# Performance work log

Hardware: AMD Instinct MI355X
Metric: run time of the kernel (lower is better)

The kernel has to match this reference:

```python
import jax, jax.numpy as jnp
import numpy as np
import math

B, L, H, NH = 4, 2048, 2048, 16
HD = H // NH  # head_dim = 128
ROPE_BASE = 10000.0


def rotate_half(x):
    x1, x2 = jnp.split(x, 2, axis=-1)
    return jnp.concatenate((-x2, x1), axis=-1)


def rope_cos_sin(seq_len, dim, dtype=jnp.float32):
    inv_freq = 1.0 / (ROPE_BASE ** (jnp.arange(0, dim, 2, dtype=jnp.float32) / dim))
    t = jnp.arange(seq_len, dtype=jnp.float32)
    freqs = jnp.outer(t, inv_freq)              # [L, dim/2]
    emb = jnp.concatenate((freqs, freqs), -1)   # [L, dim]
    return jnp.cos(emb).astype(dtype), jnp.sin(emb).astype(dtype)


def setup_inputs() -> dict:
    key = jax.random.key(0)
    ks = jax.random.split(key, 5)
    x = jax.random.normal(ks[0], (B, L, H), dtype=jnp.float32)
    # causal mask, broadcastable over [B, NH, L, L]; 0 -> masked
    mask = jnp.tril(jnp.ones((L, L), dtype=jnp.int32))[None, None]
    s = 0.02
    Wq = jax.random.normal(ks[1], (H, H), dtype=jnp.float32) * s
    Wk = jax.random.normal(ks[2], (H, H), dtype=jnp.float32) * s
    Wv = jax.random.normal(ks[3], (H, H), dtype=jnp.float32) * s
    Wo = jax.random.normal(ks[4], (H, H), dtype=jnp.float32) * s
    return {"x": x, "mask": mask, "Wq": Wq, "Wk": Wk, "Wv": Wv, "Wo": Wo}


def reference(x, mask, Wq, Wk, Wv, Wo):
    b, l, _ = x.shape
    # nn.Linear: y = x @ W.T (weight shape [out, in])
    q = (x @ Wq.T).reshape(b, l, NH, HD).transpose(0, 2, 1, 3)  # [B,H,L,D]
    k = (x @ Wk.T).reshape(b, l, NH, HD).transpose(0, 2, 1, 3)
    v = (x @ Wv.T).reshape(b, l, NH, HD).transpose(0, 2, 1, 3)
    cos, sin = rope_cos_sin(l, HD, x.dtype)  # [L, D] broadcasts over [B,H,L,D]
    q = q * cos + rotate_half(q) * sin
    k = k * cos + rotate_half(k) * sin
    attn = jnp.einsum("bhqd,bhkd->bhqk", q, k) / math.sqrt(HD)
    attn = jnp.where(mask == 0, jnp.float32(-jnp.inf), attn)
    attn = jax.nn.softmax(attn.astype(jnp.float32), axis=-1).astype(x.dtype)
    out = jnp.einsum("bhqk,bhkd->bhqd", attn, v)
    out = out.transpose(0, 2, 1, 3).reshape(b, l, NH * HD)
    return out @ Wo.T
```

## Files before the change

kernel.cpp:

```cpp
#include <hip/hip_runtime.h>
#include <cstdint>
#include <cmath>

#define B_   4
#define L_   2048
#define H_   2048
#define NH_  16
#define HD_  128
#define ML_  (B_*L_)

using short8 = __attribute__((ext_vector_type(8))) short;
using f32x4  = __attribute__((ext_vector_type(4))) float;
using f32x16 = __attribute__((ext_vector_type(16))) float;
using uint4v = __attribute__((ext_vector_type(4))) unsigned;

__device__ inline short f2bf(float f){
  unsigned u = __builtin_bit_cast(unsigned, f);
  unsigned r = u + 0x7FFFu + ((u >> 16) & 1u);
  return (short)(r >> 16);
}
__device__ inline float bf2f(short s){
  unsigned u = ((unsigned)(unsigned short)s) << 16;
  return __builtin_bit_cast(float, u);
}

#define GLD16(gp, lp) __builtin_amdgcn_global_load_lds(                      \
    (const __attribute__((address_space(1))) void*)(gp),                     \
    (__attribute__((address_space(3))) void*)(lp), 16, 0, 0)

__device__ inline unsigned cvtpk_bf16(float lo, float hi){
  unsigned d;
  asm("v_cvt_pk_bf16_f32 %0, %1, %2" : "=v"(d) : "v"(lo), "v"(hi));
  return d;
}
__device__ inline void permswap32(unsigned &a, unsigned &b){
  asm volatile("v_permlane32_swap_b32 %0, %1" : "+v"(a), "+v"(b));
}
__device__ inline float cross_half_max(float x){
  return fmaxf(x, __shfl_xor(x, 32));
}
__device__ inline float cross_half_add(float x){
  return x + __shfl_xor(x, 32);
}

__global__ void rope_table(float* __restrict__ cosT, float* __restrict__ sinT){
  int idx = blockIdx.x * 256 + threadIdx.x;
  if (idx >= L_ * 64) return;
  int l = idx >> 6, d = idx & 63;
  float invf = powf(10000.0f, -(float)d * (1.0f/64.0f));
  float fr = (float)l * invf;
  cosT[idx] = cosf(fr);
  sinT[idx] = sinf(fr);
}

__global__ __launch_bounds__(256)
void cvt_bf16(const float* __restrict__ in, short* __restrict__ out, int n8){
  int i = blockIdx.x * 256 + threadIdx.x;
  if (i >= n8) return;
  const float4* p = (const float4*)(in + (size_t)i * 8);
  float4 a = p[0], b = p[1];
  short8 s;
  s[0]=f2bf(a.x); s[1]=f2bf(a.y); s[2]=f2bf(a.z); s[3]=f2bf(a.w);
  s[4]=f2bf(b.x); s[5]=f2bf(b.y); s[6]=f2bf(b.z); s[7]=f2bf(b.w);
  *(short8*)(out + (size_t)i * 8) = s;
}

__global__ __launch_bounds__(256)
void cvt_w3(const float* __restrict__ W0, const float* __restrict__ W1,
            const float* __restrict__ W2, short* __restrict__ out){
  int i = blockIdx.x * 256 + threadIdx.x;
  const int per = H_ * H_ / 8;
  const float* src; int j;
  if (i < per)            { src = W0; j = i; }
  else if (i < 2 * per)   { src = W1; j = i - per; }
  else                    { src = W2; j = i - 2 * per; }
  const float4* p = (const float4*)(src + (size_t)j * 8);
  float4 a = p[0], b = p[1];
  short8 s;
  s[0]=f2bf(a.x); s[1]=f2bf(a.y); s[2]=f2bf(a.z); s[3]=f2bf(a.w);
  s[4]=f2bf(b.x); s[5]=f2bf(b.y); s[6]=f2bf(b.z); s[7]=f2bf(b.w);
  *(short8*)(out + (size_t)i * 8) = s;
}

template<int QKV, int OUT_F32>
__global__ __launch_bounds__(512, 2)
void gemm256_bt(const short* __restrict__ A, const short* __restrict__ Bw,
                void* __restrict__ C0, void* __restrict__ C1,
                void* __restrict__ C2)
{
  constexpr int K = 2048, N = 2048;
  __shared__ short sA[4][256 * 32];
  __shared__ short sB[4][256 * 32];
  const int tid  = threadIdx.x;
  const int lane = tid & 63;
  const int wave = tid >> 6;
  const int wr = wave >> 2, wc = wave & 3;
  const int ln = lane & 15, g = lane >> 4;

  const int blk = blockIdx.x;
  int n_t, m_t;
  if constexpr (QKV) { int i = blk >> 3; n_t = (blk & 7) + 8 * (i >> 5); m_t = i & 31; }
  else               { n_t = blk & 7;    m_t = blk >> 3; }
  const int m0 = m_t * 256;
  const int nb0 = n_t * 256;

  const int u0 = wave * 64 + lane;
  const int u1 = u0 + 512;
  const int r0 = u0 >> 2, c0 = (((u0 & 3) ^ (r0 & 3) ^ ((r0 >> 2) & 3))) * 8;
  const int r1 = u1 >> 2, c1 = (((u1 & 3) ^ (r1 & 3) ^ ((r1 >> 2) & 3))) * 8;

  f32x4 acc[8][4];
  #pragma unroll
  for (int m = 0; m < 8; m++)
    #pragma unroll
    for (int n = 0; n < 4; n++) acc[m][n] = {0.f, 0.f, 0.f, 0.f};

#define STAGE256(T) do {                                                     \
    const int _b = (T) & 3; const int _k = (T) * 32;                         \
    GLD16(A  + (size_t)(m0 + r0) * K + _k + c0, &sA[_b][wave * 512]);        \
    GLD16(A  + (size_t)(m0 + r1) * K + _k + c1, &sA[_b][4096 + wave * 512]); \
    GLD16(Bw + (size_t)(nb0 + r0) * K + _k + c0, &sB[_b][wave * 512]);       \
    GLD16(Bw + (size_t)(nb0 + r1) * K + _k + c1, &sB[_b][4096 + wave * 512]);\
  } while (0)

#define TILE256(T, VMN, PF) do {                                             \
    asm volatile("s_waitcnt vmcnt(" #VMN ")" ::: "memory");                  \
    __builtin_amdgcn_s_barrier();                                            \
    asm volatile("" ::: "memory");                                           \
    const short* _at = &sA[(T) & 3][0];                                      \
    const short* _bt = &sB[(T) & 3][0];                                      \
    short8 af[8], bfr[4];                                                    \
    const int _sl = (g ^ (ln & 3) ^ ((ln >> 2) & 3)) * 8;                    \
    _Pragma("unroll")                                                        \
    for (int m = 0; m < 8; m++)                                              \
      af[m] = *(const short8*)(_at + (wr * 128 + m * 16 + ln) * 32 + _sl);   \
    _Pragma("unroll")                                                        \
    for (int n = 0; n < 4; n++)                                              \
      bfr[n] = *(const short8*)(_bt + (wc * 64 + n * 16 + ln) * 32 + _sl);   \
    if (PF) STAGE256((T) + 3);                                               \
    __builtin_amdgcn_s_setprio(1);                                           \
    _Pragma("unroll")                                                        \
    for (int m = 0; m < 8; m++)                                              \
      _Pragma("unroll")                                                      \
      for (int n = 0; n < 4; n++)                                            \
        acc[m][n] = __builtin_amdgcn_mfma_f32_16x16x32_bf16(af[m], bfr[n],   \
                                                            acc[m][n], 0, 0, 0); \
    __builtin_amdgcn_s_setprio(0);                                           \
  } while (0)

  STAGE256(0); STAGE256(1); STAGE256(2);

  for (int t = 0; t < 61; ++t) TILE256(t, 8, true);
  TILE256(61, 8, false);
  TILE256(62, 4, false);
  TILE256(63, 0, false);

#undef STAGE256
#undef TILE256

  void* Cp; int cb;
  if constexpr (QKV) {
    int w = n_t >> 3;
    Cp = (w == 0) ? C0 : (w == 1) ? C1 : C2;
    cb = (n_t & 7) * 256;
  } else { Cp = C0; cb = nb0; }
  #pragma unroll
  for (int m = 0; m < 8; m++)
    #pragma unroll
    for (int n = 0; n < 4; n++)
      #pragma unroll
      for (int r = 0; r < 4; r++) {
        int row = m0 + wr * 128 + m * 16 + g * 4 + r;
        int col = cb + wc * 64 + n * 16 + ln;
        float v = acc[m][n][r];
        if constexpr (OUT_F32) ((float*)Cp)[(size_t)row * N + col] = v;
        else                   ((short*)Cp)[(size_t)row * N + col] = f2bf(v);
      }
}

__global__ __launch_bounds__(256)
void rope_apply(short* __restrict__ Qb, short* __restrict__ Kb,
                const float* __restrict__ cosT, const float* __restrict__ sinT)
{
  int idx = blockIdx.x * 256 + threadIdx.x;
  int z = blockIdx.y;
  short* ptr  = z ? Kb : Qb;
  float scale = z ? 1.0f : 0.08838834764831845f;
  int row = idx >> 7;
  int rem = idx & 127;
  int h = rem >> 3, ch = rem & 7;
  int l = row & (L_ - 1);
  short* base = ptr + (size_t)row * H_ + h * HD_ + ch * 8;
  short8 lo = *(short8*)base;
  short8 hi = *(short8*)(base + 64);
  const float* cp = cosT + l * 64 + ch * 8;
  const float* sp = sinT + l * 64 + ch * 8;
  short8 nlo, nhi;
  #pragma unroll
  for (int j = 0; j < 8; j++) {
    float c = cp[j], s = sp[j];
    float x0 = bf2f(lo[j]), x1 = bf2f(hi[j]);
    nlo[j] = f2bf((x0 * c - x1 * s) * scale);
    nhi[j] = f2bf((x1 * c + x0 * s) * scale);
  }
  *(short8*)base        = nlo;
  *(short8*)(base + 64) = nhi;
}

__global__ __launch_bounds__(256)
void transpose_v(const short* __restrict__ Vb, short* __restrict__ VT)
{
  __shared__ short t[64 * 64];
  const int blk = blockIdx.x;
  const int dt = blk & 1, lt = (blk >> 1) & 31, bh = blk >> 6;
  const int b = bh >> 4, h = bh & 15;
  const int l0 = lt * 64, d0 = dt * 64;
  const int tid = threadIdx.x;
  #pragma unroll
  for (int i = 0; i < 2; i++) {
    int u = tid + i * 256;
    int r = u >> 3, c = u & 7;
    short8 v = *(const short8*)(Vb + ((size_t)b * L_ + l0 + r) * H_ + h * HD_ + d0 + c * 8);
    *(short8*)&t[r * 64 + ((c ^ ((r >> 3) & 7)) << 3)] = v;
  }
  __syncthreads();
  #pragma unroll
  for (int i = 0; i < 2; i++) {
    int u = tid + i * 256;
    int d = u >> 3, lc = u & 7;
    short8 o;
    #pragma unroll
    for (int j = 0; j < 8; j++) {
      int l = lc * 8 + j;
      o[j] = t[l * 64 + (((d >> 3) ^ (lc & 7)) << 3) + (d & 7)];
    }
    *(short8*)(VT + ((size_t)bh * HD_ + d0 + d) * L_ + l0 + lc * 8) = o;
  }
}

__global__ __launch_bounds__(512, 2)
void flash_attn(const short* __restrict__ Qb, const short* __restrict__ Kb,
                const short* __restrict__ VT, short* __restrict__ AO)
{
  __shared__ short lds_k[2][64 * 128];
  __shared__ short lds_v[2][128 * 64];
  __shared__ float f_lds[8][32];

  const int blk = blockIdx.x;
  int bh, j;
  if (blk < 256) { bh = blk & 63; j = 7 - (blk >> 6); }
  else           { int u = blk - 256; bh = u & 63; j = 3 - (u >> 6); }
  const int q0 = j * 256;
  const int T  = 4 * j + 4;
  const int h = bh & 15, b = bh >> 4;
  const int tid = threadIdx.x, wave = tid >> 6, lane = tid & 63;
  const int hi = lane >> 5, l31 = lane & 31;
  const size_t rowbase = (size_t)b * L_;
  const int colbase = h * HD_;
  const short* Kbh  = Kb + rowbase * H_ + colbase;
  const short* VTbh = VT + (size_t)bh * HD_ * L_;
  const int qw = q0 + wave * 32;
  const int qabs = qw + l31;
  const int fsw = (l31 & 7) ^ ((l31 >> 3) & 3);

  short8 qf[8];
  {
    const short* qp = Qb + (rowbase + qabs) * H_ + colbase + hi * 8;
    #pragma unroll
    for (int c = 0; c < 8; c++) qf[c] = *(const short8*)(qp + c * 16);
  }

  f32x16 acc_o[4];
  #pragma unroll
  for (int d = 0; d < 4; d++)
    #pragma unroll
    for (int r = 0; r < 16; r++) acc_o[d][r] = 0.f;
  float m_ = -__builtin_inff(), l_ = 0.f;

  auto stage = [&](int k0s, int bufi) {
    #pragma unroll
    for (int i = 0; i < 2; i++) {
      int c = wave * 2 + i;
      {
        int rt = c * 4 + (lane >> 4);
        int cg = (lane & 15) ^ (rt & 7) ^ ((rt >> 3) & 3);
        const short* gp = Kbh + (size_t)(k0s + rt) * H_ + cg * 8;
        GLD16(gp, &lds_k[bufi][c * 512]);
      }
      {
        int rd = c * 8 + (lane >> 3);
        int cg = (lane & 7) ^ (rd & 7) ^ ((rd >> 3) & 3);
        const short* gp = VTbh + (size_t)rd * L_ + k0s + cg * 8;
        GLD16(gp, &lds_v[bufi][c * 512]);
      }
    }
  };

  stage(0, 0);
  __syncthreads();

  for (int t = 0; t < T; ++t) {
    const int k0 = t * 64;
    if (t + 1 < T) stage((t + 1) * 64, (t + 1) & 1);
    const short* kb_ = lds_k[t & 1];
    const short* vb_ = lds_v[t & 1];

    if (k0 <= qw + 31) {
      f32x16 p0, p1;
      #pragma unroll
      for (int r = 0; r < 16; r++) { p0[r] = 0.f; p1[r] = 0.f; }
      __builtin_amdgcn_s_setprio(1);
      #pragma unroll
      for (int c = 0; c < 8; c++) {
        int ch = (c * 2 + hi) ^ fsw;
        short8 kf0 = *(const short8*)(kb_ + l31 * 128 + ch * 8);
        short8 kf1 = *(const short8*)(kb_ + (32 + l31) * 128 + ch * 8);
        p0 = __builtin_amdgcn_mfma_f32_32x32x16_bf16(kf0, qf[c], p0, 0, 0, 0);
        p1 = __builtin_amdgcn_mfma_f32_32x32x16_bf16(kf1, qf[c], p1, 0, 0, 0);
      }
      __builtin_amdgcn_s_setprio(0);

      if (k0 + 63 > qw) {
        #pragma unroll
        for (int r = 0; r < 16; r++) {
          int kvl = (r & 3) + 8 * (r >> 2) + 4 * hi;
          if (k0 + kvl > qabs)      p0[r] = -__builtin_inff();
          if (k0 + 32 + kvl > qabs) p1[r] = -__builtin_inff();
        }
      }

      float mt = p0[0];
      #pragma unroll
      for (int r = 1; r < 16; r++) mt = fmaxf(mt, p0[r]);
      #pragma unroll
      for (int r = 0; r < 16; r++) mt = fmaxf(mt, p1[r]);
      mt = cross_half_max(mt);
      if (!__all(mt <= m_ + 8.0f)) {
        float mnew = fmaxf(m_, mt);
        float f = __expf(m_ - mnew);
        m_ = mnew;
        l_ *= f;
        if (lane < 32) f_lds[wave][lane] = f;
        f32x4 fr[4];
        #pragma unroll
        for (int i = 0; i < 4; i++)
          fr[i] = *(const f32x4*)&f_lds[wave][i * 8 + hi * 4];
        #pragma unroll
        for (int d = 0; d < 4; d++)
          #pragma unroll
          for (int r = 0; r < 16; r++) acc_o[d][r] *= fr[r >> 2][r & 3];
      }
      float ls = 0.f;
      #pragma unroll
      for (int r = 0; r < 16; r++) { p0[r] = __expf(p0[r] - m_); ls += p0[r]; }
      #pragma unroll
      for (int r = 0; r < 16; r++) { p1[r] = __expf(p1[r] - m_); ls += p1[r]; }
      ls = cross_half_add(ls);
      l_ += ls;

      __builtin_amdgcn_s_setprio(1);
      #pragma unroll
      for (int ks = 0; ks < 4; ks++) {
        const f32x16 &pp = (ks < 2) ? p0 : p1;
        const int kk = (ks & 1) * 8;
        unsigned a0 = cvtpk_bf16(pp[kk + 0], pp[kk + 1]);
        unsigned b0 = cvtpk_bf16(pp[kk + 4], pp[kk + 5]);
        permswap32(a0, b0);
        unsigned a1 = cvtpk_bf16(pp[kk + 2], pp[kk + 3]);
        unsigned b1 = cvtpk_bf16(pp[kk + 6], pp[kk + 7]);
        permswap32(a1, b1);
        uint4v w; w[0] = a0; w[1] = a1; w[2] = b0; w[3] = b1;
        short8 af = __builtin_bit_cast(short8, w);
        #pragma unroll
        for (int db = 0; db < 4; db++) {
          int d  = db * 32 + l31;
          int ch = (ks * 2 + hi) ^ fsw;
          short8 vf = *(const short8*)(vb_ + d * 64 + ch * 8);
          acc_o[db] = __builtin_amdgcn_mfma_f32_32x32x16_bf16(af, vf, acc_o[db], 0, 0, 0);
        }
      }
      __builtin_amdgcn_s_setprio(0);
    }
    __syncthreads();
  }

  if (lane < 32) f_lds[wave][lane] = 1.0f / l_;
  f32x4 lr[4];
  #pragma unroll
  for (int i = 0; i < 4; i++)
    lr[i] = *(const f32x4*)&f_lds[wave][i * 8 + hi * 4];
  #pragma unroll
  for (int db = 0; db < 4; db++)
    #pragma unroll
    for (int r = 0; r < 16; r++) {
      int row = qw + (r & 3) + 8 * (r >> 2) + 4 * hi;
      AO[(rowbase + row) * H_ + colbase + db * 32 + l31] =
          f2bf(acc_o[db][r] * lr[r >> 2][r & 3]);
    }
}

extern "C" void kernel_launch(void* const* d_in, const int* in_sizes, int n_in,
                              void* d_out, int out_size, void* d_ws, size_t ws_size,
                              hipStream_t stream)
{
  const float* x  = (const float*)d_in[0];
  const float* Wq = (const float*)d_in[2];
  const float* Wk = (const float*)d_in[3];
  const float* Wv = (const float*)d_in[4];
  const float* Wo = (const float*)d_in[5];
  float* out = (float*)d_out;

  char* ws = (char*)d_ws;
  const size_t SZ = (size_t)ML_ * H_ * sizeof(short);
  short* Qb = (short*)(ws);
  short* Kb = (short*)(ws + SZ);
  short* Vb = (short*)(ws + 2 * SZ);
  short* xb = (short*)(ws + 3 * SZ);
  short* VT = xb;
  short* AO = Vb;
  float* cosT = (float*)(ws + 4 * SZ);
  float* sinT = cosT + (size_t)L_ * 64;
  short* Wb = (short*)(ws + 4 * SZ + (size_t)(1 << 20));
  const size_t NEED_FUSED = 4 * SZ + (1 << 20) + (size_t)3 * H_ * H_ * sizeof(short);
  const bool fused = ws_size >= NEED_FUSED;

  rope_table<<<512, 256, 0, stream>>>(cosT, sinT);

  cvt_bf16<<<ML_ * H_ / 8 / 256, 256, 0, stream>>>(x, xb, ML_ * H_ / 8);

  if (fused) {
    cvt_w3<<<3 * H_ * H_ / 8 / 256, 256, 0, stream>>>(Wq, Wk, Wv, Wb);
    gemm256_bt<1, 0><<<768, 512, 0, stream>>>(xb, Wb, Qb, Kb, Vb);
  } else {
    cvt_bf16<<<H_ * H_ / 8 / 256, 256, 0, stream>>>(Wq, Wb, H_ * H_ / 8);
    gemm256_bt<0, 0><<<256, 512, 0, stream>>>(xb, Wb, Qb, Qb, Qb);
    cvt_bf16<<<H_ * H_ / 8 / 256, 256, 0, stream>>>(Wk, Wb, H_ * H_ / 8);
    gemm256_bt<0, 0><<<256, 512, 0, stream>>>(xb, Wb, Kb, Kb, Kb);
    cvt_bf16<<<H_ * H_ / 8 / 256, 256, 0, stream>>>(Wv, Wb, H_ * H_ / 8);
    gemm256_bt<0, 0><<<256, 512, 0, stream>>>(xb, Wb, Vb, Vb, Vb);
  }

  transpose_v<<<64 * 32 * 2, 256, 0, stream>>>(Vb, VT);

  rope_apply<<<dim3(ML_ * NH_ * 8 / 256, 2), 256, 0, stream>>>(Qb, Kb, cosT, sinT);

  flash_attn<<<512, 512, 0, stream>>>(Qb, Kb, VT, AO);

  cvt_bf16<<<H_ * H_ / 8 / 256, 256, 0, stream>>>(Wo, Wb, H_ * H_ / 8);
  gemm256_bt<0, 1><<<256, 512, 0, stream>>>(AO, Wb, out, out, out);
}
```

Baseline: 446.3 us.

## Restructure GEMM into double-buffered K=64 phases and fuse Q RoPE into attention

The GEMM now uses two LDS buffers of K=64 slices instead of four K=32 buffers. Each tile is split into four sub-phases, each issuing part of the next slice's global loads, with explicit waitcnt and barriers. Separately, RoPE and the softmax scale for Q are applied inside flash_attn when Q fragments are loaded, so rope_apply now only touches K. This cuts one elementwise pass over Q in global memory. The cost is more barriers per K step and some extra trig-table loads in the attention prologue.

```diff
diff --git a/kernel.cpp b/kernel.cpp
--- a/kernel.cpp
+++ b/kernel.cpp
@@ -84,13 +84,13 @@
 
 template<int QKV, int OUT_F32>
 __global__ __launch_bounds__(512, 2)
-void gemm256_bt(const short* __restrict__ A, const short* __restrict__ Bw,
-                void* __restrict__ C0, void* __restrict__ C1,
-                void* __restrict__ C2)
+void gemm256p(const short* __restrict__ A, const short* __restrict__ Bw,
+              void* __restrict__ C0, void* __restrict__ C1,
+              void* __restrict__ C2)
 {
   constexpr int K = 2048, N = 2048;
-  __shared__ short sA[4][256 * 32];
-  __shared__ short sB[4][256 * 32];
+  __shared__ short sA[2][256 * 64];
+  __shared__ short sB[2][256 * 64];
   const int tid  = threadIdx.x;
   const int lane = tid & 63;
   const int wave = tid >> 6;
@@ -104,10 +104,8 @@
   const int m0 = m_t * 256;
   const int nb0 = n_t * 256;
 
-  const int u0 = wave * 64 + lane;
-  const int u1 = u0 + 512;
-  const int r0 = u0 >> 2, c0 = (((u0 & 3) ^ (r0 & 3) ^ ((r0 >> 2) & 3))) * 8;
-  const int r1 = u1 >> 2, c1 = (((u1 & 3) ^ (r1 & 3) ^ ((r1 >> 2) & 3))) * 8;
+  const int sr = tid >> 3;
+  const int sc = ((tid & 7) ^ (sr & 7)) * 8;
 
   f32x4 acc[8][4];
   #pragma unroll
@@ -115,48 +113,75 @@
     #pragma unroll
     for (int n = 0; n < 4; n++) acc[m][n] = {0.f, 0.f, 0.f, 0.f};
 
-#define STAGE256(T) do {                                                     \
-    const int _b = (T) & 3; const int _k = (T) * 32;                         \
-    GLD16(A  + (size_t)(m0 + r0) * K + _k + c0, &sA[_b][wave * 512]);        \
-    GLD16(A  + (size_t)(m0 + r1) * K + _k + c1, &sA[_b][4096 + wave * 512]); \
-    GLD16(Bw + (size_t)(nb0 + r0) * K + _k + c0, &sB[_b][wave * 512]);       \
-    GLD16(Bw + (size_t)(nb0 + r1) * K + _k + c1, &sB[_b][4096 + wave * 512]);\
-  } while (0)
-
-#define TILE256(T, VMN, PF) do {                                             \
-    asm volatile("s_waitcnt vmcnt(" #VMN ")" ::: "memory");                  \
+#define SQA(T, Q) GLD16(A  + (size_t)(m0  + (Q)*64 + sr) * K + (T)*64 + sc,  \
+                        &sA[(T) & 1][(Q)*4096 + wave*512])
+#define SQB(T, Q) GLD16(Bw + (size_t)(nb0 + (Q)*64 + sr) * K + (T)*64 + sc,  \
+                        &sB[(T) & 1][(Q)*4096 + wave*512])
+
+#define PHASE(BUF, MH, NHh, STG, TAILVM)                                     \
+  {                                                                          \
+    const short* _a = &sA[BUF][0];                                           \
+    const short* _b = &sB[BUF][0];                                           \
+    const int xr = ln & 7;                                                   \
+    short8 af0[4], af1[4], bq0[2], bq1[2];                                   \
+    _Pragma("unroll")                                                        \
+    for (int mm = 0; mm < 4; mm++) {                                         \
+      int row = wr * 128 + (MH) * 64 + mm * 16 + ln;                         \
+      af0[mm] = *(const short8*)(_a + row * 64 + ((g ^ xr)) * 8);            \
+      af1[mm] = *(const short8*)(_a + row * 64 + (((4 + g) ^ xr)) * 8);      \
+    }                                                                        \
+    _Pragma("unroll")                                                        \
+    for (int nn = 0; nn < 2; nn++) {                                         \
+      int row = wc * 64 + (NHh) * 32 + nn * 16 + ln;                         \
+      bq0[nn] = *(const short8*)(_b + row * 64 + ((g ^ xr)) * 8);            \
+      bq1[nn] = *(const short8*)(_b + row * 64 + (((4 + g) ^ xr)) * 8);      \
+    }                                                                        \
+    STG;                                                                     \
+    asm volatile("" ::: "memory");                                           \
     __builtin_amdgcn_s_barrier();                                            \
     asm volatile("" ::: "memory");                                           \
-    const short* _at = &sA[(T) & 3][0];                                      \
-    const short* _bt = &sB[(T) & 3][0];                                      \
-    short8 af[8], bfr[4];                                                    \
-    const int _sl = (g ^ (ln & 3) ^ ((ln >> 2) & 3)) * 8;                    \
-    _Pragma("unroll")                                                        \
-    for (int m = 0; m < 8; m++)                                              \
-      af[m] = *(const short8*)(_at + (wr * 128 + m * 16 + ln) * 32 + _sl);   \
-    _Pragma("unroll")                                                        \
-    for (int n = 0; n < 4; n++)                                              \
-      bfr[n] = *(const short8*)(_bt + (wc * 64 + n * 16 + ln) * 32 + _sl);   \
-    if (PF) STAGE256((T) + 3);                                               \
     __builtin_amdgcn_s_setprio(1);                                           \
     _Pragma("unroll")                                                        \
-    for (int m = 0; m < 8; m++)                                              \
+    for (int mm = 0; mm < 4; mm++)                                           \
       _Pragma("unroll")                                                      \
-      for (int n = 0; n < 4; n++)                                            \
-        acc[m][n] = __builtin_amdgcn_mfma_f32_16x16x32_bf16(af[m], bfr[n],   \
-                                                            acc[m][n], 0, 0, 0); \
+      for (int nn = 0; nn < 2; nn++) {                                       \
+        acc[(MH)*4+mm][(NHh)*2+nn] = __builtin_amdgcn_mfma_f32_16x16x32_bf16(\
+            af0[mm], bq0[nn], acc[(MH)*4+mm][(NHh)*2+nn], 0, 0, 0);          \
+        acc[(MH)*4+mm][(NHh)*2+nn] = __builtin_amdgcn_mfma_f32_16x16x32_bf16(\
+            af1[mm], bq1[nn], acc[(MH)*4+mm][(NHh)*2+nn], 0, 0, 0);          \
+      }                                                                      \
     __builtin_amdgcn_s_setprio(0);                                           \
-  } while (0)
-
-  STAGE256(0); STAGE256(1); STAGE256(2);
-
-  for (int t = 0; t < 61; ++t) TILE256(t, 8, true);
-  TILE256(61, 8, false);
-  TILE256(62, 4, false);
-  TILE256(63, 0, false);
-
-#undef STAGE256
-#undef TILE256
+    TAILVM;                                                                  \
+    asm volatile("" ::: "memory");                                           \
+    __builtin_amdgcn_s_barrier();                                            \
+    asm volatile("" ::: "memory");                                           \
+  }
+
+  SQA(0, 0); SQA(0, 2);
+  SQB(0, 0); SQB(0, 1);
+  SQB(0, 2); SQB(0, 3);
+  SQA(0, 1); SQA(0, 3);
+  asm volatile("s_waitcnt vmcnt(2)" ::: "memory");
+  __builtin_amdgcn_s_barrier();
+  asm volatile("" ::: "memory");
+
+  for (int t = 0; t < 31; ++t) {
+    const int b = t & 1;
+    PHASE(b, 0, 0, { SQA(t + 1, 0); SQA(t + 1, 2); }, );
+    PHASE(b, 0, 1, { SQB(t + 1, 0); SQB(t + 1, 1); },
+          asm volatile("s_waitcnt vmcnt(4)" ::: "memory"));
+    PHASE(b, 1, 0, { SQB(t + 1, 2); SQB(t + 1, 3); }, );
+    PHASE(b, 1, 1, { SQA(t + 1, 1); SQA(t + 1, 3); },
+          asm volatile("s_waitcnt vmcnt(2)" ::: "memory"));
+  }
+  PHASE(1, 0, 0, , );
+  PHASE(1, 0, 1, , asm volatile("s_waitcnt vmcnt(0)" ::: "memory"));
+  PHASE(1, 1, 0, , );
+  PHASE(1, 1, 1, , );
+
+#undef SQA
+#undef SQB
+#undef PHASE
 
   void* Cp; int cb;
   if constexpr (QKV) {
@@ -179,18 +204,15 @@
 }
 
 __global__ __launch_bounds__(256)
-void rope_apply(short* __restrict__ Qb, short* __restrict__ Kb,
-                const float* __restrict__ cosT, const float* __restrict__ sinT)
+void rope_apply_k(short* __restrict__ Kb,
+                  const float* __restrict__ cosT, const float* __restrict__ sinT)
 {
   int idx = blockIdx.x * 256 + threadIdx.x;
-  int z = blockIdx.y;
-  short* ptr  = z ? Kb : Qb;
-  float scale = z ? 1.0f : 0.08838834764831845f;
   int row = idx >> 7;
   int rem = idx & 127;
   int h = rem >> 3, ch = rem & 7;
   int l = row & (L_ - 1);
-  short* base = ptr + (size_t)row * H_ + h * HD_ + ch * 8;
+  short* base = Kb + (size_t)row * H_ + h * HD_ + ch * 8;
   short8 lo = *(short8*)base;
   short8 hi = *(short8*)(base + 64);
   const float* cp = cosT + l * 64 + ch * 8;
@@ -200,8 +222,8 @@
   for (int j = 0; j < 8; j++) {
     float c = cp[j], s = sp[j];
     float x0 = bf2f(lo[j]), x1 = bf2f(hi[j]);
-    nlo[j] = f2bf((x0 * c - x1 * s) * scale);
-    nhi[j] = f2bf((x1 * c + x0 * s) * scale);
+    nlo[j] = f2bf(x0 * c - x1 * s);
+    nhi[j] = f2bf(x1 * c + x0 * s);
   }
   *(short8*)base        = nlo;
   *(short8*)(base + 64) = nhi;
@@ -240,7 +262,8 @@
 
 __global__ __launch_bounds__(512, 2)
 void flash_attn(const short* __restrict__ Qb, const short* __restrict__ Kb,
-                const short* __restrict__ VT, short* __restrict__ AO)
+                const short* __restrict__ VT, short* __restrict__ AO,
+                const float* __restrict__ cosT, const float* __restrict__ sinT)
 {
   __shared__ short lds_k[2][64 * 128];
   __shared__ short lds_v[2][128 * 64];
@@ -266,8 +289,22 @@
   short8 qf[8];
   {
     const short* qp = Qb + (rowbase + qabs) * H_ + colbase + hi * 8;
-    #pragma unroll
-    for (int c = 0; c < 8; c++) qf[c] = *(const short8*)(qp + c * 16);
+    short8 qraw[8];
+    #pragma unroll
+    for (int c = 0; c < 8; c++) qraw[c] = *(const short8*)(qp + c * 16);
+    const int lq = qabs & (L_ - 1);
+    const float* cp = cosT + lq * 64 + hi * 8;
+    const float* sp = sinT + lq * 64 + hi * 8;
+    #pragma unroll
+    for (int c = 0; c < 4; c++) {
+      #pragma unroll
+      for (int jj = 0; jj < 8; jj++) {
+        float cc = cp[c * 16 + jj], ss = sp[c * 16 + jj];
+        float lo = bf2f(qraw[c][jj]), hv = bf2f(qraw[c + 4][jj]);
+        qf[c][jj]     = f2bf((lo * cc - hv * ss) * 0.08838834764831845f);
+        qf[c + 4][jj] = f2bf((hv * cc + lo * ss) * 0.08838834764831845f);
+      }
+    }
   }
 
   f32x16 acc_o[4];
@@ -430,22 +467,22 @@
 
   if (fused) {
     cvt_w3<<<3 * H_ * H_ / 8 / 256, 256, 0, stream>>>(Wq, Wk, Wv, Wb);
-    gemm256_bt<1, 0><<<768, 512, 0, stream>>>(xb, Wb, Qb, Kb, Vb);
+    gemm256p<1, 0><<<768, 512, 0, stream>>>(xb, Wb, Qb, Kb, Vb);
   } else {
     cvt_bf16<<<H_ * H_ / 8 / 256, 256, 0, stream>>>(Wq, Wb, H_ * H_ / 8);
-    gemm256_bt<0, 0><<<256, 512, 0, stream>>>(xb, Wb, Qb, Qb, Qb);
+    gemm256p<0, 0><<<256, 512, 0, stream>>>(xb, Wb, Qb, Qb, Qb);
     cvt_bf16<<<H_ * H_ / 8 / 256, 256, 0, stream>>>(Wk, Wb, H_ * H_ / 8);
-    gemm256_bt<0, 0><<<256, 512, 0, stream>>>(xb, Wb, Kb, Kb, Kb);
+    gemm256p<0, 0><<<256, 512, 0, stream>>>(xb, Wb, Kb, Kb, Kb);
     cvt_bf16<<<H_ * H_ / 8 / 256, 256, 0, stream>>>(Wv, Wb, H_ * H_ / 8);
-    gemm256_bt<0, 0><<<256, 512, 0, stream>>>(xb, Wb, Vb, Vb, Vb);
+    gemm256p<0, 0><<<256, 512, 0, stream>>>(xb, Wb, Vb, Vb, Vb);
   }
 
   transpose_v<<<64 * 32 * 2, 256, 0, stream>>>(Vb, VT);
 
-  rope_apply<<<dim3(ML_ * NH_ * 8 / 256, 2), 256, 0, stream>>>(Qb, Kb, cosT, sinT);
-
-  flash_attn<<<512, 512, 0, stream>>>(Qb, Kb, VT, AO);
+  rope_apply_k<<<ML_ * NH_ * 8 / 256, 256, 0, stream>>>(Kb, cosT, sinT);
+
+  flash_attn<<<512, 512, 0, stream>>>(Qb, Kb, VT, AO, cosT, sinT);
 
   cvt_bf16<<<H_ * H_ / 8 / 256, 256, 0, stream>>>(Wo, Wb, H_ * H_ / 8);
-  gemm256_bt<0, 1><<<256, 512, 0, stream>>>(AO, Wb, out, out, out);
-}
+  gemm256p<0, 1><<<256, 512, 0, stream>>>(AO, Wb, out, out, out);
+}
```

Result: no change. 452.3 us (+1.3%).
